# Kernel optimization log

Measured on AMD Instinct MI355X. Metric: run time of the kernel, lower is better.

## Reference

```python
import jax, jax.numpy as jnp
import numpy as np


def setup_inputs() -> dict:
    key = jax.random.key(0)
    k1, k2, k3, k4 = jax.random.split(key, 4)
    B, d, C, O = 8, 32768, 128, 128
    x = jax.random.normal(k1, (B, d, C), dtype=jnp.float32)
    alpha = jax.random.normal(k2, (C, O), dtype=jnp.float32)
    beta = jax.random.normal(k3, (C, O), dtype=jnp.float32)
    bias = jax.random.normal(k4, (C, O), dtype=jnp.float32)
    return {"x": x, "alpha": alpha, "beta": beta, "bias": bias}


def reference(x, alpha, beta, bias):
    # Original: mean over C of x[...,None]*alpha + x_sum[...,None]*beta + bias
    # Algebraic factorization: (x @ alpha + x_sum @ beta) / C + mean(bias, axis=0)
    C = x.shape[-1]
    x_sum = jnp.sum(x, axis=1, keepdims=True)          # (B, 1, C)
    term_a = jnp.einsum('bdc,co->bdo', x, alpha)        # (B, d, O)
    term_b = jnp.einsum('bdc,co->bdo', x_sum, beta)     # (B, 1, O)
    bias_mean = jnp.mean(bias, axis=0)                  # (O,)
    return (term_a + term_b) / C + bias_mean
```

## Files before the change

### kernel.cpp

```cpp
#include <hip/hip_runtime.h>
#include <hip/hip_bf16.h>

static constexpr int BB = 8;
static constexpr int DD = 32768;
static constexpr int CC = 128;
static constexpr int OO = 128;

typedef __attribute__((ext_vector_type(8))) short short8;
typedef __attribute__((ext_vector_type(4))) float f32x4;

__global__ __launch_bounds__(256) void colsum_k(const float* __restrict__ x,
                                                const float* __restrict__ alpha,
                                                float* __restrict__ part,
                                                ushort* __restrict__ alphaT) {
    int blk = blockIdx.x;
    int t = threadIdx.x;
    if (blk >= 1024) {
        int e = (blk - 1024) * 1024 + t * 4;
        #pragma unroll
        for (int j = 0; j < 4; ++j) {
            int g = e + j;
            int o = g >> 7, c = g & 127;
            __hip_bfloat16 h = __float2bfloat16(alpha[c * OO + o]);
            alphaT[g] = *reinterpret_cast<ushort*>(&h);
        }
        return;
    }
    int b = blk >> 7, chunk = blk & 127;
    long base = ((long)b * DD + (long)chunk * 256) * CC;
    int c4 = t & 31, rg = t >> 5;
    f32x4 acc = {0.f, 0.f, 0.f, 0.f};
    const float* xp = x + base + c4 * 4;
    for (int r = rg; r < 256; r += 8) {
        float4 v = *reinterpret_cast<const float4*>(xp + (long)r * CC);
        acc[0] += v.x; acc[1] += v.y; acc[2] += v.z; acc[3] += v.w;
    }
    __shared__ f32x4 red[256];
    red[t] = acc;
    __syncthreads();
    if (t < 32) {
        f32x4 s = red[t];
        #pragma unroll
        for (int g = 1; g < 8; ++g) {
            f32x4 v = red[t + g * 32];
            s[0] += v[0]; s[1] += v[1]; s[2] += v[2]; s[3] += v[3];
        }
        *reinterpret_cast<f32x4*>(part + blk * CC + t * 4) = s;
    }
}

__global__ __launch_bounds__(256) void addvec_k(const float* __restrict__ part,
                                                const float* __restrict__ beta,
                                                const float* __restrict__ bias,
                                                float* __restrict__ add) {
    int b = blockIdx.x;
    int t = threadIdx.x;
    int c = t & 127, half = t >> 7;
    __shared__ float xs2[2][128];
    __shared__ float xsum[128];
    float s = 0.f;
    for (int ch = half * 64; ch < half * 64 + 64; ++ch)
        s += part[(b * 128 + ch) * CC + c];
    xs2[half][c] = s;
    __syncthreads();
    if (t < 128) xsum[t] = xs2[0][t] + xs2[1][t];
    __syncthreads();
    float a = 0.f;
    for (int cc = half * 64; cc < half * 64 + 64; ++cc)
        a += xsum[cc] * beta[cc * OO + c] + bias[cc * OO + c];
    xs2[half][c] = a;
    __syncthreads();
    if (t < 128) add[b * OO + t] = (xs2[0][t] + xs2[1][t]) * (1.0f / (float)CC);
}

#define LSTR 136
__global__ __launch_bounds__(256) void gemm_k(const float* __restrict__ x,
                                              const ushort* __restrict__ alphaT,
                                              const float* __restrict__ add,
                                              float* __restrict__ out) {
    __shared__ ushort a_sh[128 * LSTR];
    __shared__ float add_sh[BB * OO];
    int t = threadIdx.x;
    #pragma unroll
    for (int i = 0; i < 8; ++i) {
        int ci = i * 256 + t;
        int o = ci >> 4, cseg = (ci & 15) * 8;
        short8 v = *reinterpret_cast<const short8*>(alphaT + o * CC + cseg);
        *reinterpret_cast<short8*>(&a_sh[o * LSTR + cseg]) = v;
    }
    *reinterpret_cast<float4*>(&add_sh[t * 4]) = *reinterpret_cast<const float4*>(add + t * 4);
    __syncthreads();

    int w = t >> 6, l = t & 63;
    int lr = l & 15, kq = l >> 4;
    int wid = blockIdx.x * 4 + w;
    const float inv = 1.0f / (float)CC;

    for (int it = 0; it < 4; ++it) {
        int tile = wid + it * 4096;
        long base = (long)tile * 16 * CC;
        int b = tile >> 11;
        f32x4 xv[8];
        const float* xp = x + base + lr * CC + kq * 8;
        #pragma unroll
        for (int kk = 0; kk < 4; ++kk) {
            xv[kk * 2]     = *reinterpret_cast<const f32x4*>(xp + kk * 32);
            xv[kk * 2 + 1] = *reinterpret_cast<const f32x4*>(xp + kk * 32 + 4);
        }
        f32x4 acc[8];
        #pragma unroll
        for (int n = 0; n < 8; ++n) acc[n] = {0.f, 0.f, 0.f, 0.f};
        #pragma unroll
        for (int kk = 0; kk < 4; ++kk) {
            short8 af;
            #pragma unroll
            for (int j = 0; j < 4; ++j) {
                __hip_bfloat16 h0 = __float2bfloat16(xv[kk * 2][j]);
                af[j] = *reinterpret_cast<short*>(&h0);
                __hip_bfloat16 h1 = __float2bfloat16(xv[kk * 2 + 1][j]);
                af[4 + j] = *reinterpret_cast<short*>(&h1);
            }
            #pragma unroll
            for (int n = 0; n < 8; ++n) {
                short8 bf = *reinterpret_cast<const short8*>(
                    &a_sh[(n * 16 + lr) * LSTR + kk * 32 + kq * 8]);
                acc[n] = __builtin_amdgcn_mfma_f32_16x16x32_bf16(bf, af, acc[n], 0, 0, 0);
            }
        }
        #pragma unroll
        for (int n = 0; n < 8; ++n) {
            int o0 = n * 16 + kq * 4;
            float4 ad = *reinterpret_cast<const float4*>(&add_sh[b * OO + o0]);
            float4 v;
            v.x = acc[n][0] * inv + ad.x;
            v.y = acc[n][1] * inv + ad.y;
            v.z = acc[n][2] * inv + ad.z;
            v.w = acc[n][3] * inv + ad.w;
            *reinterpret_cast<float4*>(out + base + (long)lr * OO + o0) = v;
        }
    }
}

extern "C" void kernel_launch(void* const* d_in, const int* in_sizes, int n_in,
                              void* d_out, int out_size, void* d_ws, size_t ws_size,
                              hipStream_t stream) {
    const float* x     = (const float*)d_in[0];
    const float* alpha = (const float*)d_in[1];
    const float* beta  = (const float*)d_in[2];
    const float* bias  = (const float*)d_in[3];
    float* out = (float*)d_out;

    float*  part   = (float*)d_ws;
    ushort* alphaT = (ushort*)((char*)d_ws + 524288);
    float*  add    = (float*)((char*)d_ws + 557056);

    colsum_k<<<1040, 256, 0, stream>>>(x, alpha, part, alphaT);
    addvec_k<<<8,    256, 0, stream>>>(part, beta, bias, add);
    gemm_k<<<1024,   256, 0, stream>>>(x, alphaT, add, out);
}
```

Measured before the change: 264.3 us.

## Fuse colsum, addvec and GEMM into one cooperative kernel with grid syncs

After: 693.1 us. 2.62x slower.

```diff
diff --git a/kernel.cpp b/kernel.cpp
--- a/kernel.cpp
+++ b/kernel.cpp
@@ -1,5 +1,8 @@
 #include <hip/hip_runtime.h>
 #include <hip/hip_bf16.h>
+#include <hip/hip_cooperative_groups.h>
+
+namespace cg = cooperative_groups;
 
 static constexpr int BB = 8;
 static constexpr int DD = 32768;
@@ -8,6 +11,128 @@
 
 typedef __attribute__((ext_vector_type(8))) short short8;
 typedef __attribute__((ext_vector_type(4))) float f32x4;
+
+#define LSTR 136
+
+__device__ __forceinline__ ushort f2bf(float f) {
+    __hip_bfloat16 h = __float2bfloat16(f);
+    return *reinterpret_cast<ushort*>(&h);
+}
+
+__global__ __launch_bounds__(256, 4) void fused_k(
+    const float* __restrict__ x, const float* __restrict__ alpha,
+    const float* __restrict__ beta, const float* __restrict__ bias,
+    float* __restrict__ part, float* __restrict__ add, float* __restrict__ out) {
+    __shared__ __align__(16) ushort a_sh[128 * LSTR];
+    __shared__ float add_sh[BB * OO];
+    __shared__ float xsum_sh[128];
+    int blk = blockIdx.x, t = threadIdx.x;
+
+    {
+        int b = blk >> 7, chunk = blk & 127;
+        long base = ((long)b * DD + (long)chunk * 256) * CC;
+        int c4 = t & 31, rg = t >> 5;
+        f32x4 acc = {0.f, 0.f, 0.f, 0.f};
+        const float* xp = x + base + c4 * 4;
+        for (int r = rg; r < 256; r += 8) {
+            float4 v = *reinterpret_cast<const float4*>(xp + (long)r * CC);
+            acc[0] += v.x; acc[1] += v.y; acc[2] += v.z; acc[3] += v.w;
+        }
+        f32x4* red = reinterpret_cast<f32x4*>(a_sh);
+        red[t] = acc;
+        __syncthreads();
+        if (t < 32) {
+            f32x4 s = red[t];
+            #pragma unroll
+            for (int g = 1; g < 8; ++g) {
+                f32x4 v = red[t + g * 32];
+                s[0] += v[0]; s[1] += v[1]; s[2] += v[2]; s[3] += v[3];
+            }
+            *reinterpret_cast<f32x4*>(part + blk * CC + t * 4) = s;
+        }
+        __syncthreads();
+    }
+    #pragma unroll
+    for (int i = 0; i < 16; ++i) {
+        int q = i * 256 + t;
+        int c = q >> 5, o4 = (q & 31) * 4;
+        float4 v = *reinterpret_cast<const float4*>(alpha + c * OO + o4);
+        a_sh[(o4 + 0) * LSTR + c] = f2bf(v.x);
+        a_sh[(o4 + 1) * LSTR + c] = f2bf(v.y);
+        a_sh[(o4 + 2) * LSTR + c] = f2bf(v.z);
+        a_sh[(o4 + 3) * LSTR + c] = f2bf(v.w);
+    }
+    __threadfence();
+    cg::this_grid().sync();
+
+    if (blk < BB) {
+        int c = t & 127, half = t >> 7;
+        float s = 0.f;
+        for (int ch = half * 64; ch < half * 64 + 64; ++ch)
+            s += part[(blk * 128 + ch) * CC + c];
+        add_sh[half * 128 + c] = s;
+        __syncthreads();
+        if (t < 128) xsum_sh[t] = add_sh[t] + add_sh[128 + t];
+        __syncthreads();
+        float a = 0.f;
+        for (int cc = half * 64; cc < half * 64 + 64; ++cc)
+            a += xsum_sh[cc] * beta[cc * OO + c] + bias[cc * OO + c];
+        add_sh[half * 128 + c] = a;
+        __syncthreads();
+        if (t < 128) add[blk * OO + t] = (add_sh[t] + add_sh[128 + t]) * (1.0f / (float)CC);
+    }
+    __threadfence();
+    cg::this_grid().sync();
+
+    *reinterpret_cast<float4*>(&add_sh[t * 4]) = *reinterpret_cast<const float4*>(add + t * 4);
+    __syncthreads();
+
+    int w = t >> 6, l = t & 63;
+    int lr = l & 15, kq = l >> 4;
+    const float inv = 1.0f / (float)CC;
+
+    for (int it = 0; it < 4; ++it) {
+        int tile = blk * 16 + it * 4 + w;
+        long base = (long)tile * 16 * CC;
+        int b = tile >> 11;
+        f32x4 xv[8];
+        const float* xp = x + base + lr * CC + kq * 8;
+        #pragma unroll
+        for (int kk = 0; kk < 4; ++kk) {
+            xv[kk * 2]     = *reinterpret_cast<const f32x4*>(xp + kk * 32);
+            xv[kk * 2 + 1] = *reinterpret_cast<const f32x4*>(xp + kk * 32 + 4);
+        }
+        f32x4 acc[8];
+        #pragma unroll
+        for (int n = 0; n < 8; ++n) acc[n] = {0.f, 0.f, 0.f, 0.f};
+        #pragma unroll
+        for (int kk = 0; kk < 4; ++kk) {
+            short8 af;
+            #pragma unroll
+            for (int j = 0; j < 4; ++j) {
+                af[j]     = f2bf(xv[kk * 2][j]);
+                af[4 + j] = f2bf(xv[kk * 2 + 1][j]);
+            }
+            #pragma unroll
+            for (int n = 0; n < 8; ++n) {
+                short8 bf = *reinterpret_cast<const short8*>(
+                    &a_sh[(n * 16 + lr) * LSTR + kk * 32 + kq * 8]);
+                acc[n] = __builtin_amdgcn_mfma_f32_16x16x32_bf16(bf, af, acc[n], 0, 0, 0);
+            }
+        }
+        #pragma unroll
+        for (int n = 0; n < 8; ++n) {
+            int o0 = n * 16 + kq * 4;
+            float4 ad = *reinterpret_cast<const float4*>(&add_sh[b * OO + o0]);
+            float4 v;
+            v.x = acc[n][0] * inv + ad.x;
+            v.y = acc[n][1] * inv + ad.y;
+            v.z = acc[n][2] * inv + ad.z;
+            v.w = acc[n][3] * inv + ad.w;
+            *reinterpret_cast<float4*>(out + base + (long)lr * OO + o0) = v;
+        }
+    }
+}
 
 __global__ __launch_bounds__(256) void colsum_k(const float* __restrict__ x,
                                                 const float* __restrict__ alpha,
@@ -21,8 +146,7 @@
         for (int j = 0; j < 4; ++j) {
             int g = e + j;
             int o = g >> 7, c = g & 127;
-            __hip_bfloat16 h = __float2bfloat16(alpha[c * OO + o]);
-            alphaT[g] = *reinterpret_cast<ushort*>(&h);
+            alphaT[g] = f2bf(alpha[c * OO + o]);
         }
         return;
     }
@@ -73,12 +197,11 @@
     if (t < 128) add[b * OO + t] = (xs2[0][t] + xs2[1][t]) * (1.0f / (float)CC);
 }
 
-#define LSTR 136
 __global__ __launch_bounds__(256) void gemm_k(const float* __restrict__ x,
                                               const ushort* __restrict__ alphaT,
                                               const float* __restrict__ add,
                                               float* __restrict__ out) {
-    __shared__ ushort a_sh[128 * LSTR];
+    __shared__ __align__(16) ushort a_sh[128 * LSTR];
     __shared__ float add_sh[BB * OO];
     int t = threadIdx.x;
     #pragma unroll
@@ -115,10 +238,8 @@
             short8 af;
             #pragma unroll
             for (int j = 0; j < 4; ++j) {
-                __hip_bfloat16 h0 = __float2bfloat16(xv[kk * 2][j]);
-                af[j] = *reinterpret_cast<short*>(&h0);
-                __hip_bfloat16 h1 = __float2bfloat16(xv[kk * 2 + 1][j]);
-                af[4 + j] = *reinterpret_cast<short*>(&h1);
+                af[j]     = f2bf(xv[kk * 2][j]);
+                af[4 + j] = f2bf(xv[kk * 2 + 1][j]);
             }
             #pragma unroll
             for (int n = 0; n < 8; ++n) {
@@ -151,10 +272,16 @@
     float* out = (float*)d_out;
 
     float*  part   = (float*)d_ws;
-    ushort* alphaT = (ushort*)((char*)d_ws + 524288);
-    float*  add    = (float*)((char*)d_ws + 557056);
-
-    colsum_k<<<1040, 256, 0, stream>>>(x, alpha, part, alphaT);
-    addvec_k<<<8,    256, 0, stream>>>(part, beta, bias, add);
-    gemm_k<<<1024,   256, 0, stream>>>(x, alphaT, add, out);
-}
+    float*  add    = (float*)((char*)d_ws + 524288);
+    ushort* alphaT = (ushort*)((char*)d_ws + 528384);
+
+    void* args[] = {(void*)&x, (void*)&alpha, (void*)&beta, (void*)&bias,
+                    (void*)&part, (void*)&add, (void*)&out};
+    hipError_t e = hipLaunchCooperativeKernel((const void*)fused_k, dim3(1024), dim3(256),
+                                              args, 0, stream);
+    if (e != hipSuccess) {
+        colsum_k<<<1040, 256, 0, stream>>>(x, alpha, part, alphaT);
+        addvec_k<<<8,    256, 0, stream>>>(part, beta, bias, add);
+        gemm_k<<<1024,   256, 0, stream>>>(x, alphaT, add, out);
+    }
+}
```
